# Kernel optimization log

Measured on AMD Instinct MI355X. Metric: run time of the kernel, lower is better.

The kernel has to match this reference:

```python
import jax, jax.numpy as jnp
import numpy as np

D = 128      # memory_dim
L = 64       # segment_len
SCALE = 1.0 / np.sqrt(D)
LN_EPS = 1e-5


def _layernorm(x, g, b):
    mu = x.mean(-1, keepdims=True)
    var = ((x - mu) ** 2).mean(-1, keepdims=True)
    return (x - mu) * jax.lax.rsqrt(var + LN_EPS) * g + b


def setup_inputs() -> dict:
    key = jax.random.key(0)
    ks = jax.random.split(key, 8)
    B, T, Hd = 4, 4096, 2048
    w = 0.02  # init scale for weight matrices
    return {
        "H": jax.random.normal(ks[0], (B, T, Hd), jnp.float32),
        "M": jax.random.normal(ks[1], (B, D, D), jnp.float32),  # [B,K=128,D=128]
        "ln_g": jnp.ones((Hd,), jnp.float32),
        "ln_b": jnp.zeros((Hd,), jnp.float32),
        "W_eta_w": jax.random.normal(ks[2], (Hd,), jnp.float32) * w,
        "W_eta_b": jnp.full((1,), -5.0, jnp.float32),
        "sum_q": jax.random.normal(ks[3], (D,), jnp.float32),
        "sp_w": jax.random.normal(ks[4], (Hd, D), jnp.float32) * w,
        "sp_b": jnp.zeros((D,), jnp.float32),
        "eta_ch": jnp.ones((D,), jnp.float32),
        "temp": jnp.ones((1,), jnp.float32),
        "W_qkv": jax.random.normal(ks[5], (Hd, 3 * D), jnp.float32) * w,
    }


def reference(H, M, ln_g, ln_b, W_eta_w, W_eta_b, sum_q, sp_w, sp_b, eta_ch, temp, W_qkv):
    B, T, _ = H.shape
    K = M.shape[1]
    S = T // L  # T chosen divisible by segment_len (no-pad branch)

    Hn = _layernorm(H, ln_g, ln_b)                      # [B,T,Hd]

    # ---- write_memory ----
    H_mem = Hn @ sp_w + sp_b                            # [B,T,D]
    eta_tokens = jnp.einsum('bth,h->bt', Hn, W_eta_w) + W_eta_b  # [B,T]

    H_segs = H_mem.reshape(B, S, L, D)
    summary_scores = jnp.einsum('d,bsld->bsl', sum_q, H_segs) * SCALE
    summary_w = jax.nn.softmax(summary_scores, axis=-1)
    Z_seg = jnp.einsum('bsl,bsld->bsd', summary_w, H_segs)       # [B,S,D]

    eta_sig = jax.nn.sigmoid(eta_tokens)                          # [B,T]
    eta_seg = eta_sig.reshape(B, S, L).max(axis=-1)[..., None]    # [B,S,1]

    scores = jnp.einsum('bsd,bkd->bsk', Z_seg, M) * SCALE * jnp.exp(temp)
    A = jax.nn.softmax(scores, axis=-1)                           # [B,S,K]
    DeltaM = jnp.einsum('bsk,bsd->bkd', A, Z_seg * eta_seg)       # [B,K,D]

    eta_avg = eta_seg.mean(axis=1, keepdims=True)                 # [B,1,1]
    gate = eta_avg * jax.nn.sigmoid(eta_ch)                       # [B,1,D]
    M_new = (1.0 - gate) * M + DeltaM / S

    norm_sq = jnp.sum(DeltaM ** 2) / S
    # diversity loss on M_new
    Mn = M_new / jnp.maximum(jnp.linalg.norm(M_new, axis=-1, keepdims=True), 1e-12)
    sim = jnp.einsum('bkd,bjd->bkj', Mn, Mn) * (1.0 - jnp.eye(K, dtype=M.dtype))
    div_loss = jnp.mean(sim ** 2)
    loss = norm_sq * 0.01 + div_loss * 0.1

    # ---- read_memory (from updated memory; K<=1024 -> dense softmax path) ----
    Q_r = Hn @ W_qkv[:, 2 * D:]                                   # [B,T,D]
    r_scores = jnp.einsum('btd,bkd->btk', Q_r, M_new)
    A_r = jax.nn.softmax(r_scores * 2.0, axis=-1)
    C = jnp.einsum('btk,bkd->btd', A_r, M_new)                    # [B,T,D]

    return C, loss
```

## Files before the change

### kernel.cpp

```cpp
#include <hip/hip_runtime.h>
#include <hip/hip_bf16.h>
#include <math.h>

#define HD   2048
#define DD   128
#define TT   4096
#define BB   4
#define MT   (BB*TT)
#define LSEG 64
#define SSEG 64
#define NCOL 256
#define SCALE_D 0.088388347648318447f

typedef _Float16 half8 __attribute__((ext_vector_type(8)));
typedef _Float16 half4v __attribute__((ext_vector_type(4)));
typedef float    f32x4 __attribute__((ext_vector_type(4)));

__device__ __forceinline__ float sigmf(float x){ return 1.f/(1.f+__expf(-x)); }

__device__ __forceinline__ void glds16(const void* g, void* l) {
  __builtin_amdgcn_global_load_lds(
      (const __attribute__((address_space(1))) unsigned int*)g,
      (__attribute__((address_space(3))) unsigned int*)l, 16, 0, 0);
}

__global__ void k_pre(const float* __restrict__ ln_g, const float* __restrict__ ln_b,
                      const float* __restrict__ sp_w, const float* __restrict__ sp_b,
                      const float* __restrict__ W_qkv, const float* __restrict__ W_eta_w,
                      const float* __restrict__ W_eta_b,
                      _Float16* __restrict__ Bp, float* __restrict__ s_vec,
                      float* __restrict__ cb_vec, float* __restrict__ we2,
                      float* __restrict__ scal)
{
  __shared__ float red1[256], red2[256];
  int n = blockIdx.x, t = threadIdx.x;
  float sp = 0.f, cp = 0.f;
  if (n < NCOL) {
    for (int h = t; h < HD; h += 256) {
      float w = (n < DD) ? sp_w[(size_t)h*DD + n] : W_qkv[(size_t)h*384 + 256 + (n-DD)];
      float g = ln_g[h], b = ln_b[h];
      Bp[(size_t)n*HD + h] = (_Float16)(g*w);
      sp += g*w; cp += b*w;
    }
  } else {
    for (int h = t; h < HD; h += 256) {
      float w = W_eta_w[h];
      float g = ln_g[h], b = ln_b[h];
      we2[h] = g*w;
      sp += g*w; cp += b*w;
    }
  }
  red1[t] = sp; red2[t] = cp;
  __syncthreads();
  for (int o = 128; o > 0; o >>= 1) {
    if (t < o) { red1[t] += red1[t+o]; red2[t] += red2[t+o]; }
    __syncthreads();
  }
  if (t == 0) {
    if (n < NCOL) {
      s_vec[n]  = red1[0];
      cb_vec[n] = red2[0] + ((n < DD) ? sp_b[n] : 0.f);
    } else {
      scal[0] = red1[0];
      scal[1] = red2[0] + W_eta_b[0];
      scal[2] = 0.f; scal[3] = 0.f;
    }
  }
}

__launch_bounds__(512, 2)
__global__ void k01(const float* __restrict__ H, const _Float16* __restrict__ Bp,
                    const float* __restrict__ s_vec, const float* __restrict__ cb_vec,
                    const float* __restrict__ we2, const float* __restrict__ scal,
                    const float* __restrict__ sum_q, const float* __restrict__ Mmat,
                    const float* __restrict__ temp,
                    float* __restrict__ Q_r, float* __restrict__ Zeta,
                    float* __restrict__ A_seg, float* __restrict__ eta_seg)
{
  __shared__ __align__(16) char pool[114688];
  __shared__ float we_s[HD];
  __shared__ float smu[64], srs[64], seta[64];
  __shared__ float sq_s[128], w64_s[64], Zs[128], red_s[4];
  __shared__ float eta_sh_s;
  _Float16* sA  = (_Float16*)pool;
  _Float16* sB  = (_Float16*)(pool + 16384);
  float*    sHm = (float*)pool;

  int tid = threadIdx.x;
  int seg = blockIdx.x;
  int b   = seg >> 6;
  int m0  = seg * 64;
  int w = tid >> 6, lane = tid & 63;
  int wr = w >> 2, wc = w & 3;
  int fcol = lane & 15, kq = lane >> 4;

  for (int i = tid; i < HD/4; i += 512)
    ((float4*)we_s)[i] = ((const float4*)we2)[i];
  if (tid < 128) sq_s[tid] = sum_q[tid];
  float scal0 = scal[0], scal1 = scal[1];
  __syncthreads();

  int r_l = tid >> 3, s8 = tid & 7;
  const float* aptr = H + (size_t)(m0 + r_l)*HD + s8*8;
  int bn[4], bsl[4];
#pragma unroll
  for (int i = 0; i < 4; ++i) {
    int idx = i*512 + tid;
    bn[i]  = idx >> 3;
    bsl[i] = (idx & 7) ^ (bn[i] & 7);
  }

  f32x4 acc[2][4];
#pragma unroll
  for (int i = 0; i < 2; ++i)
#pragma unroll
    for (int j = 0; j < 4; ++j) acc[i][j] = (f32x4){0.f,0.f,0.f,0.f};
  float s1 = 0.f, s2 = 0.f, se = 0.f;

  float4 paE0 = *(const float4*)(aptr + 0);
  float4 paE1 = *(const float4*)(aptr + 4);
#pragma unroll
  for (int i = 0; i < 4; ++i)
    glds16(Bp + (size_t)bn[i]*HD + bsl[i]*8, sB + (size_t)(i*512 + tid)*8);
  float4 paO0 = *(const float4*)(aptr + 64);
  float4 paO1 = *(const float4*)(aptr + 68);
#pragma unroll
  for (int i = 0; i < 4; ++i)
    glds16(Bp + (size_t)bn[i]*HD + 64 + bsl[i]*8,
           sB + 16384 + (size_t)(i*512 + tid)*8);

  int cur3 = 0;

#define KSTEP(KT, P0, P1, VMASM, PREFETCH, BISSUE)                            \
  {                                                                           \
    _Float16* sAc = sA + ((KT)&1)*4096;                                       \
    _Float16* sBc = sB + cur3*16384;                                          \
    int k0 = (KT)*64;                                                         \
    float v[8] = {P0.x,P0.y,P0.z,P0.w, P1.x,P1.y,P1.z,P1.w};                  \
    if (PREFETCH) {                                                           \
      const float* ap_ = aptr + ((KT)+2)*64;                                  \
      P0 = *(const float4*)(ap_ + 0);                                         \
      P1 = *(const float4*)(ap_ + 4);                                         \
    }                                                                         \
    {                                                                         \
      const float4* wv4 = (const float4*)(we_s + k0 + s8*8);                  \
      float4 u0 = wv4[0], u1 = wv4[1];                                        \
      float uu[8] = {u0.x,u0.y,u0.z,u0.w, u1.x,u1.y,u1.z,u1.w};               \
      half8 h0;                                                               \
      _Pragma("unroll")                                                       \
      for (int j = 0; j < 8; ++j) {                                           \
        s1 += v[j]; s2 += v[j]*v[j]; se += v[j]*uu[j];                        \
        h0[j] = (_Float16)v[j];                                               \
      }                                                                       \
      *(half8*)&sAc[r_l*64 + (s8 ^ (r_l & 7))*8] = h0;                        \
    }                                                                         \
    asm volatile(VMASM ::: "memory");                                         \
    __builtin_amdgcn_s_barrier();                                             \
    __builtin_amdgcn_sched_barrier(0);                                        \
    if (BISSUE) {                                                             \
      int wb3 = cur3 + 2; if (wb3 >= 3) wb3 -= 3;                             \
      _Float16* sBn = sB + wb3*16384;                                         \
      const _Float16* bsrc = Bp + (k0 + 128);                                 \
      _Pragma("unroll")                                                       \
      for (int i = 0; i < 4; ++i)                                             \
        glds16(bsrc + (size_t)bn[i]*HD + bsl[i]*8,                            \
               sBn + (size_t)(i*512 + tid)*8);                                \
      __builtin_amdgcn_sched_barrier(0);                                      \
    }                                                                         \
    __builtin_amdgcn_s_setprio(1);                                            \
    _Pragma("unroll")                                                         \
    for (int ks = 0; ks < 2; ++ks) {                                          \
      half8 af[2], bf[4];                                                     \
      _Pragma("unroll")                                                       \
      for (int rt = 0; rt < 2; ++rt) {                                        \
        int r = wr*32 + rt*16 + fcol;                                         \
        int ch = (ks*4 + kq) ^ (r & 7);                                       \
        af[rt] = *(half8*)&sAc[r*64 + ch*8];                                  \
      }                                                                       \
      _Pragma("unroll")                                                       \
      for (int ct = 0; ct < 4; ++ct) {                                        \
        int n = wc*64 + ct*16 + fcol;                                         \
        int ch = (ks*4 + kq) ^ (n & 7);                                       \
        bf[ct] = *(half8*)&sBc[n*64 + ch*8];                                  \
      }                                                                       \
      _Pragma("unroll")                                                       \
      for (int rt = 0; rt < 2; ++rt)                                          \
        _Pragma("unroll")                                                     \
        for (int ct = 0; ct < 4; ++ct)                                        \
          acc[rt][ct] = __builtin_amdgcn_mfma_f32_16x16x32_f16(af[rt], bf[ct], acc[rt][ct], 0,0,0); \
    }                                                                         \
    __builtin_amdgcn_s_setprio(0);                                            \
    cur3 += 1; if (cur3 >= 3) cur3 -= 3;                                      \
  }

#pragma unroll 1
  for (int kp = 0; kp < 15; ++kp) {
    KSTEP(2*kp,   paE0, paE1, "s_waitcnt vmcnt(8) lgkmcnt(0)", 1, 1)
    KSTEP(2*kp+1, paO0, paO1, "s_waitcnt vmcnt(8) lgkmcnt(0)", 1, 1)
  }
  KSTEP(30, paE0, paE1, "s_waitcnt vmcnt(6) lgkmcnt(0)", 0, 0)
  KSTEP(31, paO0, paO1, "s_waitcnt vmcnt(0) lgkmcnt(0)", 0, 0)
#undef KSTEP

  s1 += __shfl_xor(s1, 1); s1 += __shfl_xor(s1, 2); s1 += __shfl_xor(s1, 4);
  s2 += __shfl_xor(s2, 1); s2 += __shfl_xor(s2, 2); s2 += __shfl_xor(s2, 4);
  se += __shfl_xor(se, 1); se += __shfl_xor(se, 2); se += __shfl_xor(se, 4);
  if (s8 == 0) {
    float mu   = s1 * (1.f/HD);
    float var  = s2 * (1.f/HD) - mu*mu;
    float rstd = rsqrtf(var + 1e-5f);
    smu[r_l] = mu; srs[r_l] = rstd;
    seta[r_l] = rstd*(se - mu*scal0) + scal1;
  }
  __syncthreads();

#pragma unroll
  for (int ct = 0; ct < 4; ++ct) {
    int nl = wc*64 + ct*16 + fcol;
    float sn = s_vec[nl], cbn = cb_vec[nl];
#pragma unroll
    for (int rt = 0; rt < 2; ++rt)
#pragma unroll
      for (int r = 0; r < 4; ++r) {
        int m = wr*32 + rt*16 + kq*4 + r;
        sHm[m*260 + nl] = srs[m]*(acc[rt][ct][r] - smu[m]*sn) + cbn;
      }
  }
  __syncthreads();

#pragma unroll
  for (int j = 0; j < 4; ++j) {
    int idx = j*512 + tid;
    int row = idx >> 5, c4 = (idx & 31)*4;
    *(float4*)&Q_r[(size_t)(m0 + row)*DD + c4] = *(float4*)&sHm[row*260 + 128 + c4];
  }

  if (w == 0) {
    float sc = 0.f;
    const float4* hrow = (const float4*)&sHm[lane*260];
#pragma unroll
    for (int d4 = 0; d4 < 32; ++d4) {
      float4 hv = hrow[d4];
      float4 qv = *(const float4*)&sq_s[d4*4];
      sc += hv.x*qv.x + hv.y*qv.y + hv.z*qv.z + hv.w*qv.w;
    }
    sc *= SCALE_D;
    float mx = sc;
    for (int o = 32; o > 0; o >>= 1) mx = fmaxf(mx, __shfl_xor(mx, o));
    float e = __expf(sc - mx);
    float sm = e;
    for (int o = 32; o > 0; o >>= 1) sm += __shfl_xor(sm, o);
    w64_s[lane] = e / sm;
  } else if (w == 1) {
    float ev = seta[lane];
    for (int o = 32; o > 0; o >>= 1) ev = fmaxf(ev, __shfl_xor(ev, o));
    if (lane == 0) { float es = sigmf(ev); eta_sh_s = es; eta_seg[seg] = es; }
  }
  __syncthreads();

  if (tid < 128) {
    float z = 0.f;
    for (int l = 0; l < 64; ++l) z += w64_s[l]*sHm[l*260 + tid];
    Zs[tid] = z;
    Zeta[(size_t)seg*DD + tid] = z * eta_sh_s;
  }
  __syncthreads();

  float sc2 = 0.f;
  if (tid < 128) {
    const float4* mrow = (const float4*)(Mmat + ((size_t)b*DD + tid)*DD);
#pragma unroll
    for (int d4 = 0; d4 < 32; ++d4) {
      float4 mv = mrow[d4];
      sc2 += mv.x*Zs[d4*4] + mv.y*Zs[d4*4+1] + mv.z*Zs[d4*4+2] + mv.w*Zs[d4*4+3];
    }
    sc2 *= SCALE_D * __expf(temp[0]);
    float mx = sc2;
    for (int o = 32; o > 0; o >>= 1) mx = fmaxf(mx, __shfl_xor(mx, o));
    if (lane == 0) red_s[w] = mx;
  }
  __syncthreads();
  float ev2 = 0.f;
  if (tid < 128) {
    float mx = fmaxf(red_s[0], red_s[1]);
    ev2 = __expf(sc2 - mx);
    float sm = ev2;
    for (int o = 32; o > 0; o >>= 1) sm += __shfl_xor(sm, o);
    if (lane == 0) red_s[2 + w] = sm;
  }
  __syncthreads();
  if (tid < 128) {
    float smt = red_s[2] + red_s[3];
    A_seg[(size_t)seg*DD + tid] = ev2 / smt;
  }
}

__global__ void k2b(const float* __restrict__ A_seg, const float* __restrict__ Zeta,
                    const float* __restrict__ eta_seg, const float* __restrict__ Mmat,
                    const float* __restrict__ eta_ch,
                    float* __restrict__ M_new, float* __restrict__ rns_arr,
                    float* __restrict__ scal)
{
  __shared__ float As[64][33];
  __shared__ __align__(16) float Zsl[64*128];
  __shared__ float rowp[32][8];
  __shared__ float eta_av;
  __shared__ float redb[4];
  int tid = threadIdx.x;
  int b = blockIdx.x >> 2, kq = blockIdx.x & 3;
  for (int i = tid; i < 64*32; i += 256) {
    int s = i >> 5, j = i & 31;
    As[s][j] = A_seg[((size_t)b*SSEG + s)*DD + kq*32 + j];
  }
  const float4* z4 = (const float4*)(Zeta + (size_t)b*SSEG*DD);
  float4* zs4 = (float4*)Zsl;
  for (int i = tid; i < 64*32; i += 256) zs4[i] = z4[i];
  if (tid < 64) {
    float ev = eta_seg[(size_t)b*SSEG + tid];
    for (int o=32;o>0;o>>=1) ev += __shfl_xor(ev, o);
    if (tid == 0) eta_av = ev * (1.f/SSEG);
  }
  __syncthreads();
  int kl = tid & 31, dg = tid >> 5;
  int k = kq*32 + kl, d0 = dg*16;
  float dm[16];
#pragma unroll
  for (int j=0;j<16;j++) dm[j]=0.f;
  for (int s = 0; s < 64; ++s) {
    float a = As[s][kl];
    const float* zr = &Zsl[s*128 + d0];
#pragma unroll
    for (int j=0;j<16;j++) dm[j] += a * zr[j];
  }
  float nsq = 0.f;
#pragma unroll
  for (int j=0;j<16;j++) nsq += dm[j]*dm[j];
  float eav = eta_av;
  float mn[16];
  float ss = 0.f;
#pragma unroll
  for (int j=0;j<16;j++) {
    int d = d0 + j;
    float gate = eav * sigmf(eta_ch[d]);
    float v = (1.f - gate)*Mmat[((size_t)b*DD + k)*DD + d] + dm[j]*(1.f/SSEG);
    mn[j] = v; ss += v*v;
  }
#pragma unroll
  for (int j=0;j<16;j+=4) {
    float4 v4; v4.x=mn[j]; v4.y=mn[j+1]; v4.z=mn[j+2]; v4.w=mn[j+3];
    *(float4*)&M_new[((size_t)b*DD + k)*DD + d0 + j] = v4;
  }
  rowp[kl][dg] = ss;
  for (int o=1;o<64;o<<=1) nsq += __shfl_xor(nsq, o);
  if ((tid&63)==0) redb[tid>>6] = nsq;
  __syncthreads();
  if (tid == 0) atomicAdd(&scal[2], redb[0]+redb[1]+redb[2]+redb[3]);
  if (tid < 32) {
    float t2 = 0.f;
#pragma unroll
    for (int g=0; g<8; ++g) t2 += rowp[tid][g];
    float nrm = sqrtf(t2);
    rns_arr[(size_t)b*DD + kq*32 + tid] = 1.f / fmaxf(nrm, 1e-12f);
  }
}

__global__ void k2d(const float* __restrict__ M_new, const float* __restrict__ rns_arr,
                    float* __restrict__ scal)
{
  __shared__ float kr[4][128];
  __shared__ float redb[4];
  int tid = threadIdx.x;
  int b = blockIdx.x >> 5, kq = blockIdx.x & 31;
  for (int i = tid; i < 4*128; i += 256) {
    int ki = i >> 7, d = i & 127;
    kr[ki][d] = M_new[((size_t)b*DD + kq*4 + ki)*DD + d];
  }
  __syncthreads();
  int j = tid & 127, kh = tid >> 7;
  const float* mj = &M_new[((size_t)b*DD + j)*DD];
  float rj = rns_arr[(size_t)b*DD + j];
  float dv = 0.f;
#pragma unroll
  for (int ki2 = 0; ki2 < 2; ++ki2) {
    int kil = kh*2 + ki2;
    int kk = kq*4 + kil;
    float dot = 0.f;
    for (int d = 0; d < 128; d += 4) {
      float4 a = *(const float4*)(mj + d);
      dot += a.x*kr[kil][d] + a.y*kr[kil][d+1] + a.z*kr[kil][d+2] + a.w*kr[kil][d+3];
    }
    if (kk != j) {
      float sv = dot * rj * rns_arr[(size_t)b*DD + kk];
      dv += sv*sv;
    }
  }
  for (int o=1;o<64;o<<=1) dv += __shfl_xor(dv, o);
  if ((tid&63)==0) redb[tid>>6] = dv;
  __syncthreads();
  if (tid==0) atomicAdd(&scal[3], redb[0]+redb[1]+redb[2]+redb[3]);
}

__launch_bounds__(256, 1)
__global__ void k3(const float* __restrict__ Q_r, const float* __restrict__ M_new,
                   const float* __restrict__ scal, float* __restrict__ out)
{
  __shared__ __align__(16) _Float16 Mq[128*132];
  __shared__ __align__(16) _Float16 Mt[128*136];
  __shared__ __align__(16) _Float16 Ps[64*132];
  int tid = threadIdx.x;
  int b = blockIdx.x >> 6, tile = blockIdx.x & 63;
  int t0 = tile*64;
  if (blockIdx.x == 0 && tid == 0) {
    float loss = 0.01f*(scal[2]*(1.f/SSEG)) + 0.1f*(scal[3]*(1.f/(BB*DD*DD)));
    out[(size_t)MT*DD] = loss;
  }
  const float4* m4 = (const float4*)(M_new + (size_t)b*DD*DD);
#pragma unroll
  for (int it = 0; it < 4; ++it) {
    int sb = it*256 + tid;
    int rb = sb & 31, cb = sb >> 5;
    int r0 = rb*4, c0 = cb*4;
    float a[4][4];
#pragma unroll
    for (int j = 0; j < 4; ++j) {
      float4 v = m4[(size_t)(r0+j)*32 + cb];
      a[j][0]=v.x; a[j][1]=v.y; a[j][2]=v.z; a[j][3]=v.w;
    }
#pragma unroll
    for (int j = 0; j < 4; ++j) {
      half4v h; h.x=(_Float16)a[j][0]; h.y=(_Float16)a[j][1];
                h.z=(_Float16)a[j][2]; h.w=(_Float16)a[j][3];
      *(half4v*)&Mq[(r0+j)*132 + c0] = h;
    }
#pragma unroll
    for (int j2 = 0; j2 < 4; ++j2) {
      half4v h; h.x=(_Float16)a[0][j2]; h.y=(_Float16)a[1][j2];
                h.z=(_Float16)a[2][j2]; h.w=(_Float16)a[3][j2];
      *(half4v*)&Mt[(c0+j2)*136 + r0] = h;
    }
  }
  int w = tid >> 6, lane = tid & 63;
  int fcol = lane & 15, kq = lane >> 4;
  int tokA = t0 + w*16 + fcol;
  size_t qbase = ((size_t)b*TT + tokA)*DD;
  half8 af[4];
#pragma unroll
  for (int ks = 0; ks < 4; ++ks) {
    float4 q0 = *(const float4*)&Q_r[qbase + ks*32 + kq*8];
    float4 q1 = *(const float4*)&Q_r[qbase + ks*32 + kq*8 + 4];
    half8 h;
    h[0]=(_Float16)q0.x; h[1]=(_Float16)q0.y; h[2]=(_Float16)q0.z; h[3]=(_Float16)q0.w;
    h[4]=(_Float16)q1.x; h[5]=(_Float16)q1.y; h[6]=(_Float16)q1.z; h[7]=(_Float16)q1.w;
    af[ks] = h;
  }
  __syncthreads();
  f32x4 sacc[8];
#pragma unroll
  for (int nt = 0; nt < 8; ++nt) sacc[nt] = (f32x4){0.f,0.f,0.f,0.f};
#pragma unroll
  for (int nt = 0; nt < 8; ++nt)
#pragma unroll
    for (int ks = 0; ks < 4; ++ks) {
      half8 bf = *(half8*)&Mq[(nt*16 + fcol)*132 + ks*32 + kq*8];
      sacc[nt] = __builtin_amdgcn_mfma_f32_16x16x32_f16(af[ks], bf, sacc[nt], 0,0,0);
    }
#pragma unroll
  for (int nt = 0; nt < 8; ++nt)
#pragma unroll
    for (int r = 0; r < 4; ++r) sacc[nt][r] *= 2.f;
  float mx[4], sm[4];
#pragma unroll
  for (int r = 0; r < 4; ++r) {
    float m = sacc[0][r];
#pragma unroll
    for (int nt = 1; nt < 8; ++nt) m = fmaxf(m, sacc[nt][r]);
#pragma unroll
    for (int o = 1; o < 16; o <<= 1) m = fmaxf(m, __shfl_xor(m, o));
    mx[r] = m;
  }
#pragma unroll
  for (int r = 0; r < 4; ++r) sm[r] = 0.f;
#pragma unroll
  for (int nt = 0; nt < 8; ++nt)
#pragma unroll
    for (int r = 0; r < 4; ++r) {
      float e = __expf(sacc[nt][r] - mx[r]);
      sacc[nt][r] = e; sm[r] += e;
    }
#pragma unroll
  for (int r = 0; r < 4; ++r) {
    float s = sm[r];
#pragma unroll
    for (int o = 1; o < 16; o <<= 1) s += __shfl_xor(s, o);
    sm[r] = 1.f / s;
  }
#pragma unroll
  for (int nt = 0; nt < 8; ++nt)
#pragma unroll
    for (int r = 0; r < 4; ++r) {
      int tk = w*16 + kq*4 + r;
      Ps[tk*132 + nt*16 + fcol] = (_Float16)(sacc[nt][r]*sm[r]);
    }
  __syncthreads();
  half8 pf[4];
#pragma unroll
  for (int ks = 0; ks < 4; ++ks)
    pf[ks] = *(half8*)&Ps[(w*16 + fcol)*132 + ks*32 + kq*8];
  f32x4 cacc[8];
#pragma unroll
  for (int nt = 0; nt < 8; ++nt) cacc[nt] = (f32x4){0.f,0.f,0.f,0.f};
#pragma unroll
  for (int nt = 0; nt < 8; ++nt)
#pragma unroll
    for (int ks = 0; ks < 4; ++ks) {
      half8 bf = *(half8*)&Mt[(nt*16 + fcol)*136 + ks*32 + kq*8];
      cacc[nt] = __builtin_amdgcn_mfma_f32_16x16x32_f16(pf[ks], bf, cacc[nt], 0,0,0);
    }
#pragma unroll
  for (int nt = 0; nt < 8; ++nt)
#pragma unroll
    for (int r = 0; r < 4; ++r) {
      int tk = t0 + w*16 + kq*4 + r;
      out[((size_t)b*TT + tk)*DD + nt*16 + fcol] = cacc[nt][r];
    }
}

extern "C" void kernel_launch(void* const* d_in, const int* in_sizes, int n_in,
                              void* d_out, int out_size, void* d_ws, size_t ws_size,
                              hipStream_t stream)
{
  (void)in_sizes; (void)n_in; (void)out_size; (void)ws_size;
  const float* H       = (const float*)d_in[0];
  const float* Mmat    = (const float*)d_in[1];
  const float* ln_g    = (const float*)d_in[2];
  const float* ln_b    = (const float*)d_in[3];
  const float* W_eta_w = (const float*)d_in[4];
  const float* W_eta_b = (const float*)d_in[5];
  const float* sum_q   = (const float*)d_in[6];
  const float* sp_w    = (const float*)d_in[7];
  const float* sp_b    = (const float*)d_in[8];
  const float* eta_ch  = (const float*)d_in[9];
  const float* temp    = (const float*)d_in[10];
  const float* W_qkv   = (const float*)d_in[11];
  float* out           = (float*)d_out;

  char* wsb = (char*)d_ws;
  size_t off = 0;
  auto alloc = [&](size_t bytes) -> void* {
    void* p = wsb + off;
    off = (off + bytes + 255) & ~(size_t)255;
    return p;
  };
  _Float16* Bp   = (_Float16*)alloc((size_t)NCOL*HD*2);
  float* s_vec   = (float*)alloc(NCOL*4);
  float* cb_vec  = (float*)alloc(NCOL*4);
  float* we2     = (float*)alloc(HD*4);
  float* scal    = (float*)alloc(4*4);
  float* Q_r     = (float*)alloc((size_t)MT*DD*4);
  float* Zeta    = (float*)alloc((size_t)BB*SSEG*DD*4);
  float* A_seg   = (float*)alloc((size_t)BB*SSEG*DD*4);
  float* eta_seg = (float*)alloc((size_t)BB*SSEG*4);
  float* M_new   = (float*)alloc((size_t)BB*DD*DD*4);
  float* rns_arr = (float*)alloc((size_t)BB*DD*4);

  hipLaunchKernelGGL(k_pre, dim3(NCOL+1), dim3(256), 0, stream,
                     ln_g, ln_b, sp_w, sp_b, W_qkv, W_eta_w, W_eta_b,
                     Bp, s_vec, cb_vec, we2, scal);
  hipLaunchKernelGGL(k01, dim3(MT/64), dim3(512), 0, stream,
                     H, Bp, s_vec, cb_vec, we2, scal, sum_q, Mmat, temp,
                     Q_r, Zeta, A_seg, eta_seg);
  hipLaunchKernelGGL(k2b, dim3(16), dim3(256), 0, stream,
                     A_seg, Zeta, eta_seg, Mmat, eta_ch, M_new, rns_arr, scal);
  hipLaunchKernelGGL(k2d, dim3(128), dim3(256), 0, stream,
                     M_new, rns_arr, scal);
  hipLaunchKernelGGL(k3, dim3(256), dim3(256), 0, stream,
                     Q_r, M_new, scal, out);
}
```

Measured before the change: 87.06 us.

## Split main GEMM into 128-row tiles with two-way K split and combine kernel

```diff
diff --git a/kernel.cpp b/kernel.cpp
--- a/kernel.cpp
+++ b/kernel.cpp
@@ -70,38 +70,29 @@
 
 __launch_bounds__(512, 2)
 __global__ void k01(const float* __restrict__ H, const _Float16* __restrict__ Bp,
-                    const float* __restrict__ s_vec, const float* __restrict__ cb_vec,
-                    const float* __restrict__ we2, const float* __restrict__ scal,
-                    const float* __restrict__ sum_q, const float* __restrict__ Mmat,
-                    const float* __restrict__ temp,
-                    float* __restrict__ Q_r, float* __restrict__ Zeta,
-                    float* __restrict__ A_seg, float* __restrict__ eta_seg)
+                    const float* __restrict__ we2,
+                    float* __restrict__ Cp, float* __restrict__ Sp)
 {
-  __shared__ __align__(16) char pool[114688];
-  __shared__ float we_s[HD];
-  __shared__ float smu[64], srs[64], seta[64];
-  __shared__ float sq_s[128], w64_s[64], Zs[128], red_s[4];
-  __shared__ float eta_sh_s;
+  __shared__ __align__(16) char pool[133120];
+  __shared__ float we_s[1024];
   _Float16* sA  = (_Float16*)pool;
-  _Float16* sB  = (_Float16*)(pool + 16384);
+  _Float16* sB  = (_Float16*)(pool + 32768);
   float*    sHm = (float*)pool;
 
   int tid = threadIdx.x;
-  int seg = blockIdx.x;
-  int b   = seg >> 6;
-  int m0  = seg * 64;
+  int mt = blockIdx.x & 127, kh = blockIdx.x >> 7;
+  int m0r = mt * 128;
   int w = tid >> 6, lane = tid & 63;
   int wr = w >> 2, wc = w & 3;
   int fcol = lane & 15, kq = lane >> 4;
 
-  for (int i = tid; i < HD/4; i += 512)
-    ((float4*)we_s)[i] = ((const float4*)we2)[i];
-  if (tid < 128) sq_s[tid] = sum_q[tid];
-  float scal0 = scal[0], scal1 = scal[1];
-  __syncthreads();
-
-  int r_l = tid >> 3, s8 = tid & 7;
-  const float* aptr = H + (size_t)(m0 + r_l)*HD + s8*8;
+  if (tid < 256)
+    ((float4*)we_s)[tid] = ((const float4*)(we2 + kh*1024))[tid];
+  __syncthreads();
+
+  int r_l = tid >> 2, s4 = tid & 3;
+  const float* aptr = H + (size_t)(m0r + r_l)*HD + kh*1024 + s4*16;
+  const _Float16* Bph = Bp + kh*1024;
   int bn[4], bsl[4];
 #pragma unroll
   for (int i = 0; i < 4; ++i) {
@@ -110,70 +101,78 @@
     bsl[i] = (idx & 7) ^ (bn[i] & 7);
   }
 
-  f32x4 acc[2][4];
-#pragma unroll
-  for (int i = 0; i < 2; ++i)
+  f32x4 acc[4][4];
+#pragma unroll
+  for (int i = 0; i < 4; ++i)
 #pragma unroll
     for (int j = 0; j < 4; ++j) acc[i][j] = (f32x4){0.f,0.f,0.f,0.f};
   float s1 = 0.f, s2 = 0.f, se = 0.f;
 
-  float4 paE0 = *(const float4*)(aptr + 0);
-  float4 paE1 = *(const float4*)(aptr + 4);
+  float4 qE0 = *(const float4*)(aptr + 0),  qE1 = *(const float4*)(aptr + 4);
+  float4 qE2 = *(const float4*)(aptr + 8),  qE3 = *(const float4*)(aptr + 12);
+  __builtin_amdgcn_sched_barrier(0);
 #pragma unroll
   for (int i = 0; i < 4; ++i)
-    glds16(Bp + (size_t)bn[i]*HD + bsl[i]*8, sB + (size_t)(i*512 + tid)*8);
-  float4 paO0 = *(const float4*)(aptr + 64);
-  float4 paO1 = *(const float4*)(aptr + 68);
+    glds16(Bph + (size_t)bn[i]*HD + bsl[i]*8, sB + (size_t)(i*512 + tid)*8);
+  __builtin_amdgcn_sched_barrier(0);
+  float4 qO0 = *(const float4*)(aptr + 64), qO1 = *(const float4*)(aptr + 68);
+  float4 qO2 = *(const float4*)(aptr + 72), qO3 = *(const float4*)(aptr + 76);
+  __builtin_amdgcn_sched_barrier(0);
 #pragma unroll
   for (int i = 0; i < 4; ++i)
-    glds16(Bp + (size_t)bn[i]*HD + 64 + bsl[i]*8,
+    glds16(Bph + (size_t)bn[i]*HD + 64 + bsl[i]*8,
            sB + 16384 + (size_t)(i*512 + tid)*8);
-
-  int cur3 = 0;
-
-#define KSTEP(KT, P0, P1, VMASM, PREFETCH, BISSUE)                            \
+  __builtin_amdgcn_sched_barrier(0);
+
+#define KSTEP(K0V, SAB, CURB, WB, P0, P1, P2, P3, VMASM, ISSUE)               \
   {                                                                           \
-    _Float16* sAc = sA + ((KT)&1)*4096;                                       \
-    _Float16* sBc = sB + cur3*16384;                                          \
-    int k0 = (KT)*64;                                                         \
-    float v[8] = {P0.x,P0.y,P0.z,P0.w, P1.x,P1.y,P1.z,P1.w};                  \
-    if (PREFETCH) {                                                           \
-      const float* ap_ = aptr + ((KT)+2)*64;                                  \
-      P0 = *(const float4*)(ap_ + 0);                                         \
-      P1 = *(const float4*)(ap_ + 4);                                         \
-    }                                                                         \
+    _Float16* sAc = sA + (SAB)*8192;                                          \
+    _Float16* sBc = sB + (CURB)*16384;                                        \
+    const int k0 = (K0V);                                                     \
     {                                                                         \
-      const float4* wv4 = (const float4*)(we_s + k0 + s8*8);                  \
-      float4 u0 = wv4[0], u1 = wv4[1];                                        \
-      float uu[8] = {u0.x,u0.y,u0.z,u0.w, u1.x,u1.y,u1.z,u1.w};               \
-      half8 h0;                                                               \
+      float v[16] = {P0.x,P0.y,P0.z,P0.w, P1.x,P1.y,P1.z,P1.w,                \
+                     P2.x,P2.y,P2.z,P2.w, P3.x,P3.y,P3.z,P3.w};               \
+      const float4* wv4 = (const float4*)(we_s + k0 + s4*16);                 \
+      float4 u0 = wv4[0], u1 = wv4[1], u2 = wv4[2], u3 = wv4[3];              \
+      float uu[16] = {u0.x,u0.y,u0.z,u0.w, u1.x,u1.y,u1.z,u1.w,               \
+                      u2.x,u2.y,u2.z,u2.w, u3.x,u3.y,u3.z,u3.w};              \
+      half8 h0, h1;                                                           \
       _Pragma("unroll")                                                       \
-      for (int j = 0; j < 8; ++j) {                                           \
-        s1 += v[j]; s2 += v[j]*v[j]; se += v[j]*uu[j];                        \
-        h0[j] = (_Float16)v[j];                                               \
+      for (int jj = 0; jj < 8; ++jj) {                                        \
+        s1 += v[jj]; s2 += v[jj]*v[jj]; se += v[jj]*uu[jj];                   \
+        h0[jj] = (_Float16)v[jj];                                             \
       }                                                                       \
-      *(half8*)&sAc[r_l*64 + (s8 ^ (r_l & 7))*8] = h0;                        \
+      _Pragma("unroll")                                                       \
+      for (int jj = 8; jj < 16; ++jj) {                                       \
+        s1 += v[jj]; s2 += v[jj]*v[jj]; se += v[jj]*uu[jj];                   \
+        h1[jj-8] = (_Float16)v[jj];                                           \
+      }                                                                       \
+      *(half8*)&sAc[r_l*64 + ((s4*2    ) ^ (r_l & 7))*8] = h0;                \
+      *(half8*)&sAc[r_l*64 + ((s4*2 + 1) ^ (r_l & 7))*8] = h1;                \
     }                                                                         \
     asm volatile(VMASM ::: "memory");                                         \
     __builtin_amdgcn_s_barrier();                                             \
     __builtin_amdgcn_sched_barrier(0);                                        \
-    if (BISSUE) {                                                             \
-      int wb3 = cur3 + 2; if (wb3 >= 3) wb3 -= 3;                             \
-      _Float16* sBn = sB + wb3*16384;                                         \
-      const _Float16* bsrc = Bp + (k0 + 128);                                 \
+    if (ISSUE) {                                                              \
+      _Float16* sBn = sB + (WB)*16384;                                        \
+      const _Float16* bsrc = Bph + (k0 + 128);                                \
       _Pragma("unroll")                                                       \
       for (int i = 0; i < 4; ++i)                                             \
         glds16(bsrc + (size_t)bn[i]*HD + bsl[i]*8,                            \
                sBn + (size_t)(i*512 + tid)*8);                                \
       __builtin_amdgcn_sched_barrier(0);                                      \
+      const float* ap_ = aptr + k0 + 128;                                     \
+      P0 = *(const float4*)(ap_ + 0);  P1 = *(const float4*)(ap_ + 4);        \
+      P2 = *(const float4*)(ap_ + 8);  P3 = *(const float4*)(ap_ + 12);       \
+      __builtin_amdgcn_sched_barrier(0);                                      \
     }                                                                         \
     __builtin_amdgcn_s_setprio(1);                                            \
     _Pragma("unroll")                                                         \
     for (int ks = 0; ks < 2; ++ks) {                                          \
-      half8 af[2], bf[4];                                                     \
+      half8 af[4], bf[4];                                                     \
       _Pragma("unroll")                                                       \
-      for (int rt = 0; rt < 2; ++rt) {                                        \
-        int r = wr*32 + rt*16 + fcol;                                         \
+      for (int rt = 0; rt < 4; ++rt) {                                        \
+        int r = wr*64 + rt*16 + fcol;                                         \
         int ch = (ks*4 + kq) ^ (r & 7);                                       \
         af[rt] = *(half8*)&sAc[r*64 + ch*8];                                  \
       }                                                                       \
@@ -184,60 +183,119 @@
         bf[ct] = *(half8*)&sBc[n*64 + ch*8];                                  \
       }                                                                       \
       _Pragma("unroll")                                                       \
-      for (int rt = 0; rt < 2; ++rt)                                          \
+      for (int rt = 0; rt < 4; ++rt)                                          \
         _Pragma("unroll")                                                     \
         for (int ct = 0; ct < 4; ++ct)                                        \
           acc[rt][ct] = __builtin_amdgcn_mfma_f32_16x16x32_f16(af[rt], bf[ct], acc[rt][ct], 0,0,0); \
     }                                                                         \
     __builtin_amdgcn_s_setprio(0);                                            \
-    cur3 += 1; if (cur3 >= 3) cur3 -= 3;                                      \
   }
 
 #pragma unroll 1
-  for (int kp = 0; kp < 15; ++kp) {
-    KSTEP(2*kp,   paE0, paE1, "s_waitcnt vmcnt(8) lgkmcnt(0)", 1, 1)
-    KSTEP(2*kp+1, paO0, paO1, "s_waitcnt vmcnt(8) lgkmcnt(0)", 1, 1)
-  }
-  KSTEP(30, paE0, paE1, "s_waitcnt vmcnt(6) lgkmcnt(0)", 0, 0)
-  KSTEP(31, paO0, paO1, "s_waitcnt vmcnt(0) lgkmcnt(0)", 0, 0)
+  for (int kp = 0; kp < 2; ++kp) {
+    int j0 = kp*384;
+    KSTEP(j0,       0, 0, 2, qE0,qE1,qE2,qE3, "s_waitcnt vmcnt(8) lgkmcnt(0)", 1)
+    KSTEP(j0 + 64,  1, 1, 0, qO0,qO1,qO2,qO3, "s_waitcnt vmcnt(8) lgkmcnt(0)", 1)
+    KSTEP(j0 + 128, 0, 2, 1, qE0,qE1,qE2,qE3, "s_waitcnt vmcnt(8) lgkmcnt(0)", 1)
+    KSTEP(j0 + 192, 1, 0, 2, qO0,qO1,qO2,qO3, "s_waitcnt vmcnt(8) lgkmcnt(0)", 1)
+    KSTEP(j0 + 256, 0, 1, 0, qE0,qE1,qE2,qE3, "s_waitcnt vmcnt(8) lgkmcnt(0)", 1)
+    KSTEP(j0 + 320, 1, 2, 1, qO0,qO1,qO2,qO3, "s_waitcnt vmcnt(8) lgkmcnt(0)", 1)
+  }
+  KSTEP(768, 0, 0, 2, qE0,qE1,qE2,qE3, "s_waitcnt vmcnt(8) lgkmcnt(0)", 1)
+  KSTEP(832, 1, 1, 0, qO0,qO1,qO2,qO3, "s_waitcnt vmcnt(8) lgkmcnt(0)", 1)
+  KSTEP(896, 0, 2, 1, qE0,qE1,qE2,qE3, "s_waitcnt vmcnt(8) lgkmcnt(0)", 0)
+  KSTEP(960, 1, 0, 2, qO0,qO1,qO2,qO3, "s_waitcnt vmcnt(0) lgkmcnt(0)", 0)
 #undef KSTEP
 
-  s1 += __shfl_xor(s1, 1); s1 += __shfl_xor(s1, 2); s1 += __shfl_xor(s1, 4);
-  s2 += __shfl_xor(s2, 1); s2 += __shfl_xor(s2, 2); s2 += __shfl_xor(s2, 4);
-  se += __shfl_xor(se, 1); se += __shfl_xor(se, 2); se += __shfl_xor(se, 4);
-  if (s8 == 0) {
+  __syncthreads();
+
+  s1 += __shfl_xor(s1, 1); s1 += __shfl_xor(s1, 2);
+  s2 += __shfl_xor(s2, 1); s2 += __shfl_xor(s2, 2);
+  se += __shfl_xor(se, 1); se += __shfl_xor(se, 2);
+  if (s4 == 0) {
+    float4 sv; sv.x = s1; sv.y = s2; sv.z = se; sv.w = 0.f;
+    ((float4*)Sp)[(size_t)(kh*128 + mt)*128 + r_l] = sv;
+  }
+
+#pragma unroll
+  for (int ct = 0; ct < 4; ++ct) {
+    int nl = wc*64 + ct*16 + fcol;
+#pragma unroll
+    for (int rt = 0; rt < 4; ++rt)
+#pragma unroll
+      for (int r = 0; r < 4; ++r) {
+        int m = wr*64 + rt*16 + kq*4 + r;
+        sHm[m*260 + nl] = acc[rt][ct][r];
+      }
+  }
+  __syncthreads();
+
+  size_t cbase = (size_t)(kh*128 + mt)*128*256;
+#pragma unroll
+  for (int j = 0; j < 16; ++j) {
+    int idx = j*512 + tid;
+    int row = idx >> 6, c4 = (idx & 63)*4;
+    *(float4*)&Cp[cbase + (size_t)row*256 + c4] = *(float4*)&sHm[row*260 + c4];
+  }
+}
+
+__global__ void k_comb(const float* __restrict__ Cp, const float* __restrict__ Sp,
+                       const float* __restrict__ s_vec, const float* __restrict__ cb_vec,
+                       const float* __restrict__ scal, const float* __restrict__ sum_q,
+                       const float* __restrict__ Mmat, const float* __restrict__ temp,
+                       float* __restrict__ Q_r, float* __restrict__ Zeta,
+                       float* __restrict__ A_seg, float* __restrict__ eta_seg)
+{
+  __shared__ __align__(16) float sHm[64*132];
+  __shared__ float smu_s[64], srs_s[64], seta_s[64];
+  __shared__ float sv_s[256], cb_s[256];
+  __shared__ float sq_s[128], w64_s[64], Zs[128], red_s[4];
+  __shared__ float eta_sh_s;
+  int tid = threadIdx.x;
+  int seg = blockIdx.x;
+  int mt = seg >> 1, half = seg & 1, b = seg >> 6;
+  int m0 = seg * 64;
+  float scal0 = scal[0], scal1 = scal[1];
+
+  if (tid < 64) {
+    float4 a = ((const float4*)Sp)[(size_t)mt*128 + half*64 + tid];
+    float4 c = ((const float4*)Sp)[(size_t)(128 + mt)*128 + half*64 + tid];
+    float s1 = a.x + c.x, s2 = a.y + c.y, se = a.z + c.z;
     float mu   = s1 * (1.f/HD);
     float var  = s2 * (1.f/HD) - mu*mu;
     float rstd = rsqrtf(var + 1e-5f);
-    smu[r_l] = mu; srs[r_l] = rstd;
-    seta[r_l] = rstd*(se - mu*scal0) + scal1;
-  }
-  __syncthreads();
-
-#pragma unroll
-  for (int ct = 0; ct < 4; ++ct) {
-    int nl = wc*64 + ct*16 + fcol;
-    float sn = s_vec[nl], cbn = cb_vec[nl];
-#pragma unroll
-    for (int rt = 0; rt < 2; ++rt)
-#pragma unroll
-      for (int r = 0; r < 4; ++r) {
-        int m = wr*32 + rt*16 + kq*4 + r;
-        sHm[m*260 + nl] = srs[m]*(acc[rt][ct][r] - smu[m]*sn) + cbn;
-      }
-  }
-  __syncthreads();
-
-#pragma unroll
-  for (int j = 0; j < 4; ++j) {
-    int idx = j*512 + tid;
-    int row = idx >> 5, c4 = (idx & 31)*4;
-    *(float4*)&Q_r[(size_t)(m0 + row)*DD + c4] = *(float4*)&sHm[row*260 + 128 + c4];
-  }
-
+    smu_s[tid] = mu; srs_s[tid] = rstd;
+    seta_s[tid] = rstd*(se - mu*scal0) + scal1;
+  }
+  sv_s[tid] = s_vec[tid];
+  cb_s[tid] = cb_vec[tid];
+  if (tid < 128) sq_s[tid] = sum_q[tid];
+  __syncthreads();
+
+  const float4* c0 = (const float4*)(Cp + ((size_t)mt*128 + half*64)*256);
+  const float4* c1 = (const float4*)(Cp + ((size_t)(128 + mt)*128 + half*64)*256);
+#pragma unroll
+  for (int j = 0; j < 16; ++j) {
+    int idx = j*256 + tid;
+    int row = idx >> 6, cv = idx & 63;
+    float4 v0 = c0[(size_t)row*64 + cv];
+    float4 v1 = c1[(size_t)row*64 + cv];
+    float mu = smu_s[row], rs = srs_s[row];
+    int col = cv*4;
+    float4 h;
+    h.x = rs*((v0.x+v1.x) - mu*sv_s[col+0]) + cb_s[col+0];
+    h.y = rs*((v0.y+v1.y) - mu*sv_s[col+1]) + cb_s[col+1];
+    h.z = rs*((v0.z+v1.z) - mu*sv_s[col+2]) + cb_s[col+2];
+    h.w = rs*((v0.w+v1.w) - mu*sv_s[col+3]) + cb_s[col+3];
+    if (cv < 32) *(float4*)&sHm[row*132 + col] = h;
+    else         *(float4*)&Q_r[(size_t)(m0 + row)*DD + (col - 128)] = h;
+  }
+  __syncthreads();
+
+  int w = tid >> 6, lane = tid & 63;
   if (w == 0) {
     float sc = 0.f;
-    const float4* hrow = (const float4*)&sHm[lane*260];
+    const float4* hrow = (const float4*)&sHm[lane*132];
 #pragma unroll
     for (int d4 = 0; d4 < 32; ++d4) {
       float4 hv = hrow[d4];
@@ -252,7 +310,7 @@
     for (int o = 32; o > 0; o >>= 1) sm += __shfl_xor(sm, o);
     w64_s[lane] = e / sm;
   } else if (w == 1) {
-    float ev = seta[lane];
+    float ev = seta_s[lane];
     for (int o = 32; o > 0; o >>= 1) ev = fmaxf(ev, __shfl_xor(ev, o));
     if (lane == 0) { float es = sigmf(ev); eta_sh_s = es; eta_seg[seg] = es; }
   }
@@ -260,7 +318,7 @@
 
   if (tid < 128) {
     float z = 0.f;
-    for (int l = 0; l < 64; ++l) z += w64_s[l]*sHm[l*260 + tid];
+    for (int l = 0; l < 64; ++l) z += w64_s[l]*sHm[l*132 + tid];
     Zs[tid] = z;
     Zeta[(size_t)seg*DD + tid] = z * eta_sh_s;
   }
@@ -557,6 +615,8 @@
   float* we2     = (float*)alloc(HD*4);
   float* scal    = (float*)alloc(4*4);
   float* Q_r     = (float*)alloc((size_t)MT*DD*4);
+  float* Cp      = (float*)alloc((size_t)2*128*128*256*4);
+  float* Sp      = (float*)alloc((size_t)2*128*128*16);
   float* Zeta    = (float*)alloc((size_t)BB*SSEG*DD*4);
   float* A_seg   = (float*)alloc((size_t)BB*SSEG*DD*4);
   float* eta_seg = (float*)alloc((size_t)BB*SSEG*4);
@@ -566,8 +626,10 @@
   hipLaunchKernelGGL(k_pre, dim3(NCOL+1), dim3(256), 0, stream,
                      ln_g, ln_b, sp_w, sp_b, W_qkv, W_eta_w, W_eta_b,
                      Bp, s_vec, cb_vec, we2, scal);
-  hipLaunchKernelGGL(k01, dim3(MT/64), dim3(512), 0, stream,
-                     H, Bp, s_vec, cb_vec, we2, scal, sum_q, Mmat, temp,
+  hipLaunchKernelGGL(k01, dim3(256), dim3(512), 0, stream,
+                     H, Bp, we2, Cp, Sp);
+  hipLaunchKernelGGL(k_comb, dim3(BB*SSEG), dim3(256), 0, stream,
+                     Cp, Sp, s_vec, cb_vec, scal, sum_q, Mmat, temp,
                      Q_r, Zeta, A_seg, eta_seg);
   hipLaunchKernelGGL(k2b, dim3(16), dim3(256), 0, stream,
                      A_seg, Zeta, eta_seg, Mmat, eta_ch, M_new, rns_arr, scal);
```

Result: slower. 92.40 us (+6.1%).
